# Optimization experiments

Hardware: AMD Instinct MI355X
Metric: run time of the kernel (lower is better)

## Reference

```python
import jax, jax.numpy as jnp
import numpy as np

B, L, D, H, K = 4, 2048, 1024, 16, 256
DH = D // H
SCALE = DH ** -0.5


def setup_inputs() -> dict:
    key = jax.random.key(0)
    ks = jax.random.split(key, 8)
    std = 1.0 / np.sqrt(D)
    pstd = 1.0 / np.sqrt(K)  # init_ uses last dim of (seq_len, k) tensor
    return {
        "x": jax.random.normal(ks[0], (B, L, D), dtype=jnp.float32),
        "Wq": jax.random.uniform(ks[1], (D, D), jnp.float32, -std, std),
        "Wk": jax.random.uniform(ks[2], (D, D), jnp.float32, -std, std),
        "Wv": jax.random.uniform(ks[3], (D, D), jnp.float32, -std, std),
        "proj_k": jax.random.uniform(ks[4], (L, K), jnp.float32, -pstd, pstd),
        "proj_v": jax.random.uniform(ks[5], (L, K), jnp.float32, -pstd, pstd),
        "Wo": jax.random.uniform(ks[6], (D, D), jnp.float32, -std, std),
        "bo": jax.random.uniform(ks[7], (D,), jnp.float32, -std, std),
    }


def reference(x, Wq, Wk, Wv, proj_k, proj_v, Wo, bo):
    b, l, d = x.shape
    q = x @ Wq.T                                   # [B,L,D]
    keys = jnp.einsum("bnd,nk->bkd", x @ Wk.T, proj_k)   # [B,K,D]
    vals = jnp.einsum("bnd,nk->bkd", x @ Wv.T, proj_v)   # [B,K,D]
    # faithful to original: plain reshape (B,h,L,d_h), NOT transpose-split
    q = q.reshape(b, H, l, DH)
    k = keys.reshape(b, K, H, DH).transpose(0, 2, 1, 3)  # [B,H,K,DH]
    v = vals.reshape(b, K, H, DH).transpose(0, 2, 1, 3)  # [B,H,K,DH]
    attn = jax.nn.softmax(jnp.einsum("bhld,bhkd->bhlk", q, k) * SCALE, axis=-1)
    out = jnp.einsum("bhlk,bhkd->bhld", attn, v)
    out = out.transpose(0, 2, 1, 3).reshape(b, l, d)
    return out @ Wo.T + bo
```

## Files before the change

### kernel.cpp

```cpp
#include <hip/hip_runtime.h>


typedef __attribute__((ext_vector_type(8))) short short8;
typedef __attribute__((ext_vector_type(4))) short short4_t;
typedef __attribute__((ext_vector_type(4))) float facc;

#define B_    4
#define L_    2048
#define D_    1024
#define H_    16
#define KP    256
#define DH_   64
#define SCALE_ 0.125f
#define PTS   76

__device__ __forceinline__ short f2b(float f) {
  unsigned u = __float_as_uint(f);
  unsigned r = (u + 0x7fffu + ((u >> 16) & 1u)) >> 16;
  return (short)r;
}

__device__ __forceinline__ void load16_to_lds(const short* gp, short* lp) {
  __builtin_amdgcn_global_load_lds(
      (const __attribute__((address_space(1))) void*)gp,
      (__attribute__((address_space(3))) void*)lp, 16, 0, 0);
}

__global__ __launch_bounds__(256) void prepX(
    const float* __restrict__ x,  const float* __restrict__ pk,
    const float* __restrict__ pv, const float* __restrict__ w0,
    const float* __restrict__ w1, const float* __restrict__ w2,
    const float* __restrict__ w3, short* __restrict__ xb,
    short* __restrict__ xTb, short* __restrict__ projT,
    short* __restrict__ Wb)
{
  const int z = blockIdx.z, tid = threadIdx.x;
  if (z >= 6) {
    const int bid  = blockIdx.y * 32 + blockIdx.x;
    const int widx = (z - 6) * 2 + (bid >> 10);
    const float* s = (widx == 0) ? w0 : (widx == 1) ? w1 : (widx == 2) ? w2 : w3;
    const int i = ((bid & 1023) * 256 + tid) * 4;
    float4 f = *(const float4*)(s + i);
    short4_t v; v[0] = f2b(f.x); v[1] = f2b(f.y); v[2] = f2b(f.z); v[3] = f2b(f.w);
    *(short4_t*)(Wb + (size_t)widx * 1048576 + i) = v;
    return;
  }

  __shared__ float tl[32][37];
  const int row = tid >> 3, c4 = tid & 7;

  if (z < 4) {
    const int b = z, l0 = blockIdx.y * 32, d0 = blockIdx.x * 32;
    const float* s = x + (size_t)b * L_ * D_;
    float4 f = *(const float4*)(s + (size_t)(l0 + row) * D_ + d0 + c4 * 4);
    short4_t v; v[0] = f2b(f.x); v[1] = f2b(f.y); v[2] = f2b(f.z); v[3] = f2b(f.w);
    *(short4_t*)(xb + (size_t)b * L_ * D_ + (size_t)(l0 + row) * D_ + d0 + c4 * 4) = v;
    tl[row][c4 * 4 + 0] = f.x; tl[row][c4 * 4 + 1] = f.y;
    tl[row][c4 * 4 + 2] = f.z; tl[row][c4 * 4 + 3] = f.w;
    __syncthreads();
    short4_t t;
#pragma unroll
    for (int j = 0; j < 4; j++) t[j] = f2b(tl[c4 * 4 + j][row]);
    *(short4_t*)(xTb + (size_t)b * D_ * L_ + (size_t)(d0 + row) * L_ + l0 + c4 * 4) = t;
  } else {
    if (blockIdx.x >= 8) return;
    const int sel = z - 4, l0 = blockIdx.y * 32, k0 = blockIdx.x * 32;
    const float* s = sel ? pv : pk;
    float4 f = *(const float4*)(s + (size_t)(l0 + row) * KP + k0 + c4 * 4);
    tl[row][c4 * 4 + 0] = f.x; tl[row][c4 * 4 + 1] = f.y;
    tl[row][c4 * 4 + 2] = f.z; tl[row][c4 * 4 + 3] = f.w;
    __syncthreads();
    short4_t t;
#pragma unroll
    for (int j = 0; j < 4; j++) t[j] = f2b(tl[c4 * 4 + j][row]);
    *(short4_t*)(projT + (size_t)sel * (KP * L_) + (size_t)(k0 + row) * L_ + l0 + c4 * 4) = t;
  }
}

__global__ __launch_bounds__(512, 2) void gemm8p(
    const short* __restrict__ Am, const short* __restrict__ Bm,
    const float* __restrict__ bias, float* __restrict__ C32,
    short* __restrict__ Cb, int M, int N, int K)
{
  extern __shared__ __attribute__((aligned(16))) short smem[];
  constexpr int BUF  = 24576;
  constexpr int BOFF = 16384;

  const int t = threadIdx.x, lane = t & 63, w = t >> 6;
  const int lm = lane & 15, g = lane >> 4;
  const int bm = blockIdx.x * 4 + (blockIdx.y >> 3);
  const int bn = blockIdx.y & 7;
  const int m0 = bm * 256, n0 = bn * 128;
  const int wm = (w & 3) * 64, wn = (w >> 2) * 64;

  const int srow = lane >> 2;
  const int sslot = lane & 3;

  facc acc[4][4];
  const facc fz = {0.f, 0.f, 0.f, 0.f};
#pragma unroll
  for (int i = 0; i < 4; i++)
#pragma unroll
    for (int j = 0; j < 4; j++) acc[i][j] = fz;

  auto stageA = [&](int kt, int buf, int rnd) {
    const int task = rnd * 8 + w;
    const int c = task >> 4, grp = task & 15;
    const int row = grp * 16 + srow;
    const int slot = sslot ^ ((row >> 1) & 3);
    load16_to_lds(Am + (size_t)(m0 + row) * K + kt * 64 + c * 32 + slot * 8,
                  smem + buf * BUF + c * 8192 + grp * 512);
  };
  auto stageB = [&](int kt, int buf, int rnd) {
    const int task = rnd * 8 + w;
    const int c = task >> 3, grp = task & 7;
    const int row = grp * 16 + srow;
    const int slot = sslot ^ ((row >> 1) & 3);
    load16_to_lds(Bm + (size_t)(n0 + row) * K + kt * 64 + c * 32 + slot * 8,
                  smem + buf * BUF + BOFF + c * 4096 + grp * 512);
  };

#pragma unroll
  for (int r = 0; r < 4; r++) stageA(0, 0, r);
#pragma unroll
  for (int r = 0; r < 2; r++) stageB(0, 0, r);
#pragma unroll
  for (int r = 0; r < 4; r++) stageA(1, 1, r);
#pragma unroll
  for (int r = 0; r < 2; r++) stageB(1, 1, r);
  asm volatile("s_waitcnt vmcnt(6)" ::: "memory");
  __builtin_amdgcn_sched_barrier(0);
  __builtin_amdgcn_s_barrier();

  const int T = K >> 6;
  int p = 0;
  for (int kt = 0; kt < T; kt++) {
    const int q = (p == 0) ? 2 : p - 1;
    const bool pf = (kt + 2 < T);

#pragma unroll
    for (int c = 0; c < 2; c++) {
      short8 af[4], bf[4];
      const int abase = p * BUF + c * 8192;
      const int bbase = p * BUF + BOFF + c * 4096;
#pragma unroll
      for (int mt = 0; mt < 4; mt++) {
        const int row = wm + 16 * mt + lm;
        af[mt] = *(const short8*)(smem + abase + row * 32 + ((g ^ ((row >> 1) & 3)) * 8));
      }
#pragma unroll
      for (int nt = 0; nt < 4; nt++) {
        const int row = wn + 16 * nt + lm;
        bf[nt] = *(const short8*)(smem + bbase + row * 32 + ((g ^ ((row >> 1) & 3)) * 8));
      }
      if (pf) {
        if (c == 0) { stageA(kt + 2, q, 0); stageA(kt + 2, q, 1); stageB(kt + 2, q, 0); }
        else        { stageA(kt + 2, q, 2); stageA(kt + 2, q, 3); stageB(kt + 2, q, 1); }
      }
      __builtin_amdgcn_s_barrier();
      __builtin_amdgcn_s_setprio(1);
#pragma unroll
      for (int mt = 0; mt < 4; mt++)
#pragma unroll
        for (int nt = 0; nt < 4; nt++)
          acc[mt][nt] = __builtin_amdgcn_mfma_f32_16x16x32_bf16(af[mt], bf[nt], acc[mt][nt], 0, 0, 0);
      __builtin_amdgcn_s_setprio(0);
      if (c == 0) __builtin_amdgcn_s_barrier();
    }

    if (pf) {
      asm volatile("s_waitcnt vmcnt(6)" ::: "memory");
      __builtin_amdgcn_sched_barrier(0);
    } else if (kt + 1 < T) {
      asm volatile("s_waitcnt vmcnt(0)" ::: "memory");
      __builtin_amdgcn_sched_barrier(0);
    }
    __builtin_amdgcn_s_barrier();
    p = (p == 2) ? 0 : p + 1;
  }

#pragma unroll
  for (int mt = 0; mt < 4; mt++)
#pragma unroll
    for (int r = 0; r < 4; r++) {
      const int row = m0 + wm + 16 * mt + 4 * g + r;
#pragma unroll
      for (int nt = 0; nt < 4; nt++) {
        const int col = n0 + wn + 16 * nt + lm;
        float v = acc[mt][nt][r];
        if (bias) v += bias[col];
        if (C32) C32[(size_t)row * N + col] = v;
        if (Cb)  Cb[(size_t)row * N + col] = f2b(v);
      }
    }
}

template<int TM, int TN, int NC, bool SWZ>
__global__ __launch_bounds__(256) void gemm_lds(
    const short* __restrict__ Am, const short* __restrict__ Bm,
    const float* __restrict__ bias, float* __restrict__ C32,
    short* __restrict__ Cb, short* __restrict__ CbT, int M, int N, int K,
    long aHi, long aLo, long bHi, long bLo, long cHi, long cLo, int zDiv)
{
  constexpr int MT = TM / 32, NT = TN / 32;
  __shared__ __attribute__((aligned(16))) short As[NC][TM * 32];
  __shared__ __attribute__((aligned(16))) short Bs[NC][TN * 32];
  const int t = threadIdx.x, lane = t & 63, w = t >> 6;
  const int lm = lane & 15, g = lane >> 4;
  const int z = blockIdx.z, zhi = z / zDiv, zlo = z % zDiv;
  int bm, bn;
  if (SWZ) {
    const int p = blockIdx.y * 8 + blockIdx.x;
    bn = (p >> 3) & 7;
    bm = ((p >> 6) << 3) | (p & 7);
  } else {
    bm = blockIdx.y; bn = blockIdx.x;
  }
  const int m0 = bm * TM, n0 = bn * TN;
  const int wm = (w & 1) * (TM / 2), wn = (w >> 1) * (TN / 2);

  const short* Ab = Am + zhi * aHi + zlo * aLo;
  const short* Bp = Bm + zhi * bHi + zlo * bLo;

  facc acc[MT][NT];
  const facc fz = {0.f, 0.f, 0.f, 0.f};
#pragma unroll
  for (int i = 0; i < MT; i++)
#pragma unroll
    for (int j = 0; j < NT; j++) acc[i][j] = fz;

  const int lrow = lane >> 2;
  const int lch  = (lane & 3) * 8;

  for (int k0 = 0; k0 < K; k0 += 32 * NC) {
    __syncthreads();
#pragma unroll
    for (int c = 0; c < NC; c++) {
#pragma unroll
      for (int rnd = 0; rnd < TM / 64; rnd++) {
        const int row = rnd * 64 + w * 16;
        load16_to_lds(Ab + (size_t)(m0 + row + lrow) * K + k0 + c * 32 + lch,
                      &As[c][row * 32]);
      }
#pragma unroll
      for (int rnd = 0; rnd < TN / 64; rnd++) {
        const int row = rnd * 64 + w * 16;
        load16_to_lds(Bp + (size_t)(n0 + row + lrow) * K + k0 + c * 32 + lch,
                      &Bs[c][row * 32]);
      }
    }
    __syncthreads();

#pragma unroll
    for (int c = 0; c < NC; c++) {
      short8 af[MT], bf[NT];
#pragma unroll
      for (int mt = 0; mt < MT; mt++)
        af[mt] = *(const short8*)(&As[c][(wm + 16 * mt + lm) * 32 + g * 8]);
#pragma unroll
      for (int nt = 0; nt < NT; nt++)
        bf[nt] = *(const short8*)(&Bs[c][(wn + 16 * nt + lm) * 32 + g * 8]);
#pragma unroll
      for (int mt = 0; mt < MT; mt++)
#pragma unroll
        for (int nt = 0; nt < NT; nt++)
          acc[mt][nt] = __builtin_amdgcn_mfma_f32_16x16x32_bf16(af[mt], bf[nt], acc[mt][nt], 0, 0, 0);
    }
  }

  if (CbT && zhi == 1) {
#pragma unroll
    for (int mt = 0; mt < MT; mt++) {
      const int rb = m0 + wm + 16 * mt + 4 * g;
      const size_t bb = (size_t)(rb >> 8) * (16 * 64 * 256);
      const int kp = rb & 255;
#pragma unroll
      for (int nt = 0; nt < NT; nt++) {
        const int col = n0 + wn + 16 * nt + lm;
        short4_t o4;
#pragma unroll
        for (int r = 0; r < 4; r++) o4[r] = f2b(acc[mt][nt][r]);
        *(short4_t*)(CbT + bb + (size_t)col * KP + kp) = o4;
      }
    }
    return;
  }

  const long cz = zhi * cHi + zlo * cLo;
#pragma unroll
  for (int mt = 0; mt < MT; mt++)
#pragma unroll
    for (int r = 0; r < 4; r++) {
      const int row = m0 + wm + 16 * mt + 4 * g + r;
#pragma unroll
      for (int nt = 0; nt < NT; nt++) {
        const int col = n0 + wn + 16 * nt + lm;
        float v = acc[mt][nt][r];
        if (bias) v += bias[col];
        if (C32) C32[cz + (size_t)row * N + col] = v;
        if (Cb)  Cb[cz + (size_t)row * N + col] = f2b(v);
      }
    }
}

__global__ __launch_bounds__(256) void attn_mfma(
    const short* __restrict__ xqb, const short* __restrict__ keysb,
    const short* __restrict__ vTb, short* __restrict__ out2b)
{
  __shared__ __attribute__((aligned(16))) short Kt[2][64 * 72];
  __shared__ __attribute__((aligned(16))) short Vt[2][64 * 72];
  __shared__ __attribute__((aligned(16))) short Pt[4][32 * PTS];

  const int t = threadIdx.x, lane = t & 63, w = t >> 6;
  const int lm = lane & 15, g = lane >> 4;
  const int b = blockIdx.z, h = blockIdx.y;
  const int l0w = blockIdx.x * 128 + w * 32;

  short8 aq[2][2];
#pragma unroll
  for (int mt = 0; mt < 2; mt++) {
    const int l = l0w + 16 * mt + lm;
    const short* qrow = xqb + ((size_t)b * L_ + h * 128 + (l >> 4)) * D_ + (l & 15) * DH_;
#pragma unroll
    for (int ks = 0; ks < 2; ks++)
      aq[mt][ks] = *(const short8*)(qrow + ks * 32 + g * 8);
  }

  facc accO[2][4];
  const facc fz = {0.f, 0.f, 0.f, 0.f};
#pragma unroll
  for (int mt = 0; mt < 2; mt++)
#pragma unroll
    for (int dt = 0; dt < 4; dt++) accO[mt][dt] = fz;
  float lrow[2][4];
#pragma unroll
  for (int mt = 0; mt < 2; mt++)
#pragma unroll
    for (int r = 0; r < 4; r++) lrow[mt][r] = 0.f;

  const short* Kb = keysb + (size_t)b * KP * D_ + h * DH_;
  const short* Vb = vTb + ((size_t)b * H_ + h) * DH_ * KP;

  const int srow = t >> 3, sch = (t & 7) * 8;

#pragma unroll
  for (int i = 0; i < 2; i++) {
    const int row = srow + 32 * i;
    *(short8*)(&Kt[0][row * 72 + sch]) = *(const short8*)(Kb + (size_t)row * D_ + sch);
    *(short8*)(&Vt[0][row * 72 + sch]) = *(const short8*)(Vb + (size_t)row * KP + sch);
  }
  __syncthreads();

  for (int c = 0; c < 4; c++) {
    const int bi = c & 1;

    short8 kr[2], vr[2];
    if (c < 3) {
#pragma unroll
      for (int i = 0; i < 2; i++) {
        const int row = srow + 32 * i;
        kr[i] = *(const short8*)(Kb + (size_t)((c + 1) * 64 + row) * D_ + sch);
        vr[i] = *(const short8*)(Vb + (size_t)row * KP + (c + 1) * 64 + sch);
      }
    }

    facc S[2][4];
#pragma unroll
    for (int mt = 0; mt < 2; mt++)
#pragma unroll
      for (int nt = 0; nt < 4; nt++) S[mt][nt] = fz;
#pragma unroll
    for (int ks = 0; ks < 2; ks++) {
      short8 bk[4];
#pragma unroll
      for (int nt = 0; nt < 4; nt++)
        bk[nt] = *(const short8*)(&Kt[bi][(16 * nt + lm) * 72 + ks * 32 + g * 8]);
#pragma unroll
      for (int mt = 0; mt < 2; mt++)
#pragma unroll
        for (int nt = 0; nt < 4; nt++)
          S[mt][nt] = __builtin_amdgcn_mfma_f32_16x16x32_bf16(aq[mt][ks], bk[nt], S[mt][nt], 0, 0, 0);
    }

    if (c < 3) {
#pragma unroll
      for (int i = 0; i < 2; i++) {
        const int row = srow + 32 * i;
        *(short8*)(&Kt[bi ^ 1][row * 72 + sch]) = kr[i];
        *(short8*)(&Vt[bi ^ 1][row * 72 + sch]) = vr[i];
      }
    }

#pragma unroll
    for (int mt = 0; mt < 2; mt++)
#pragma unroll
      for (int r = 0; r < 4; r++) {
        float ps = 0.f;
        const int prow = (16 * mt + 4 * g + r) * PTS;
#pragma unroll
        for (int nt = 0; nt < 4; nt++) {
          const float p = __expf(S[mt][nt][r] * SCALE_);
          ps += p;
          Pt[w][prow + 16 * nt + lm] = f2b(p);
        }
        lrow[mt][r] += ps;
      }

#pragma unroll
    for (int ks = 0; ks < 2; ks++) {
      short8 ap[2], bv[4];
#pragma unroll
      for (int mt = 0; mt < 2; mt++)
        ap[mt] = *(const short8*)(&Pt[w][(16 * mt + lm) * PTS + ks * 32 + g * 8]);
#pragma unroll
      for (int dt = 0; dt < 4; dt++)
        bv[dt] = *(const short8*)(&Vt[bi][(16 * dt + lm) * 72 + ks * 32 + g * 8]);
#pragma unroll
      for (int mt = 0; mt < 2; mt++)
#pragma unroll
        for (int dt = 0; dt < 4; dt++)
          accO[mt][dt] = __builtin_amdgcn_mfma_f32_16x16x32_bf16(ap[mt], bv[dt], accO[mt][dt], 0, 0, 0);
    }
    __syncthreads();
  }

#pragma unroll
  for (int mt = 0; mt < 2; mt++)
#pragma unroll
    for (int r = 0; r < 4; r++) {
      float ls = lrow[mt][r];
      ls += __shfl_xor(ls, 1);
      ls += __shfl_xor(ls, 2);
      ls += __shfl_xor(ls, 4);
      ls += __shfl_xor(ls, 8);
      const float inv = 1.0f / ls;
      const int l = l0w + 16 * mt + 4 * g + r;
#pragma unroll
      for (int dt = 0; dt < 4; dt++)
        out2b[((size_t)b * L_ + l) * D_ + h * DH_ + 16 * dt + lm] = f2b(accO[mt][dt][r] * inv);
    }
}

extern "C" void kernel_launch(void* const* d_in, const int* in_sizes, int n_in,
                              void* d_out, int out_size, void* d_ws, size_t ws_size,
                              hipStream_t stream)
{
  const float* x      = (const float*)d_in[0];
  const float* Wq     = (const float*)d_in[1];
  const float* Wk     = (const float*)d_in[2];
  const float* Wv     = (const float*)d_in[3];
  const float* proj_k = (const float*)d_in[4];
  const float* proj_v = (const float*)d_in[5];
  const float* Wo     = (const float*)d_in[6];
  const float* bo     = (const float*)d_in[7];
  float* out = (float*)d_out;

  short* ws     = (short*)d_ws;
  short* xqb    = ws;
  short* xTb    = xqb    + 8388608;
  short* xb     = xTb    + 8388608;
  short* out2b  = xb;
  short* Wqb    = xb     + 8388608;
  short* Wkb    = Wqb    + 1048576;
  short* Wvb    = Wkb    + 1048576;
  short* Wob    = Wvb    + 1048576;
  short* projTk = Wob    + 1048576;
  short* projTv = projTk + 524288;
  short* xk2b   = projTv + 524288;
  short* xv2b   = xk2b   + 1048576;
  short* keysb  = xv2b   + 1048576;
  short* valsb  = keysb  + 1048576;
  short* vT     = valsb  + 1048576;
  (void)Wkb; (void)Wvb; (void)projTv; (void)xv2b; (void)valsb;

  static bool attr_set = false;
  if (!attr_set) {
    (void)hipFuncSetAttribute(reinterpret_cast<const void*>(gemm8p),
                              hipFuncAttributeMaxDynamicSharedMemorySize, 147456);
    attr_set = true;
  }

  prepX<<<dim3(32, 64, 8), 256, 0, stream>>>(
      x, proj_k, proj_v, Wq, Wk, Wv, Wo, xb, xTb, projTk, Wqb);

  gemm8p<<<dim3(8, 32, 1), 512, 147456, stream>>>(
      xb, Wqb, nullptr, nullptr, xqb, 8192, 1024, 1024);

  gemm_lds<64, 64, 4, false><<<dim3(16, 4, 8), 256, 0, stream>>>(
      projTk, xTb, nullptr, nullptr, xk2b, nullptr, 256, 1024, 2048,
      524288, 0, 0, (long)D_ * L_, 1048576, 262144, 4);

  gemm_lds<64, 64, 4, false><<<dim3(16, 16, 2), 256, 0, stream>>>(
      xk2b, Wkb, nullptr, nullptr, keysb, vT, 1024, 1024, 1024,
      1048576, 0, 1048576, 0, 0, 0, 1);

  attn_mfma<<<dim3(16, 16, 4), 256, 0, stream>>>(xqb, keysb, vT, out2b);

  gemm8p<<<dim3(8, 32, 1), 512, 147456, stream>>>(
      out2b, Wob, bo, out, nullptr, 8192, 1024, 1024);
}
```

Baseline: 216.4 us.

## Replace sync-per-tile GEMM with triple-buffered prefetch pipeline and swizzled LDS

The templated LDS GEMM used for the Linformer projection and K/V GEMMs is replaced by a 64x64-tile kernel with a three-stage LDS ring buffer. Loads for tile kt+2 are issued while tile kt is computed, using explicit vmcnt waits and a single barrier per iteration. The LDS chunk slot is XOR-swizzled by row to cut bank conflicts, and s_setprio raises wave priority around the MFMA block. The hand-placed waitcnt counts and barriers add some risk of ordering mistakes.

After: 216.0 us, median of 2. No clear change (-0.2%).

```diff
diff --git a/kernel.cpp b/kernel.cpp
--- a/kernel.cpp
+++ b/kernel.cpp
@@ -195,87 +195,96 @@
     }
 }
 
-template<int TM, int TN, int NC, bool SWZ>
-__global__ __launch_bounds__(256) void gemm_lds(
+__global__ __launch_bounds__(256) void gemm_p64(
     const short* __restrict__ Am, const short* __restrict__ Bm,
     const float* __restrict__ bias, float* __restrict__ C32,
     short* __restrict__ Cb, short* __restrict__ CbT, int M, int N, int K,
     long aHi, long aLo, long bHi, long bLo, long cHi, long cLo, int zDiv)
 {
-  constexpr int MT = TM / 32, NT = TN / 32;
-  __shared__ __attribute__((aligned(16))) short As[NC][TM * 32];
-  __shared__ __attribute__((aligned(16))) short Bs[NC][TN * 32];
+  __shared__ __attribute__((aligned(16))) short smem[3 * 8192];
   const int t = threadIdx.x, lane = t & 63, w = t >> 6;
   const int lm = lane & 15, g = lane >> 4;
   const int z = blockIdx.z, zhi = z / zDiv, zlo = z % zDiv;
-  int bm, bn;
-  if (SWZ) {
-    const int p = blockIdx.y * 8 + blockIdx.x;
-    bn = (p >> 3) & 7;
-    bm = ((p >> 6) << 3) | (p & 7);
-  } else {
-    bm = blockIdx.y; bn = blockIdx.x;
-  }
-  const int m0 = bm * TM, n0 = bn * TN;
-  const int wm = (w & 1) * (TM / 2), wn = (w >> 1) * (TN / 2);
+  const int bm = blockIdx.y, bn = blockIdx.x;
+  const int m0 = bm * 64, n0 = bn * 64;
+  const int wm = (w & 1) * 32, wn = (w >> 1) * 32;
 
   const short* Ab = Am + zhi * aHi + zlo * aLo;
   const short* Bp = Bm + zhi * bHi + zlo * bLo;
 
-  facc acc[MT][NT];
+  const int srow = w * 16 + (lane >> 2);
+  const int pslot = (lane & 3) ^ ((srow >> 1) & 3);
+
+  facc acc[2][2];
   const facc fz = {0.f, 0.f, 0.f, 0.f};
 #pragma unroll
-  for (int i = 0; i < MT; i++)
-#pragma unroll
-    for (int j = 0; j < NT; j++) acc[i][j] = fz;
-
-  const int lrow = lane >> 2;
-  const int lch  = (lane & 3) * 8;
-
-  for (int k0 = 0; k0 < K; k0 += 32 * NC) {
-    __syncthreads();
-#pragma unroll
-    for (int c = 0; c < NC; c++) {
-#pragma unroll
-      for (int rnd = 0; rnd < TM / 64; rnd++) {
-        const int row = rnd * 64 + w * 16;
-        load16_to_lds(Ab + (size_t)(m0 + row + lrow) * K + k0 + c * 32 + lch,
-                      &As[c][row * 32]);
-      }
-#pragma unroll
-      for (int rnd = 0; rnd < TN / 64; rnd++) {
-        const int row = rnd * 64 + w * 16;
-        load16_to_lds(Bp + (size_t)(n0 + row + lrow) * K + k0 + c * 32 + lch,
-                      &Bs[c][row * 32]);
-      }
-    }
-    __syncthreads();
-
-#pragma unroll
-    for (int c = 0; c < NC; c++) {
-      short8 af[MT], bf[NT];
-#pragma unroll
-      for (int mt = 0; mt < MT; mt++)
-        af[mt] = *(const short8*)(&As[c][(wm + 16 * mt + lm) * 32 + g * 8]);
-#pragma unroll
-      for (int nt = 0; nt < NT; nt++)
-        bf[nt] = *(const short8*)(&Bs[c][(wn + 16 * nt + lm) * 32 + g * 8]);
-#pragma unroll
-      for (int mt = 0; mt < MT; mt++)
-#pragma unroll
-        for (int nt = 0; nt < NT; nt++)
+  for (int i = 0; i < 2; i++)
+#pragma unroll
+    for (int j = 0; j < 2; j++) acc[i][j] = fz;
+
+  auto stage_h = [&](int kt, int buf, int c) {
+    load16_to_lds(Ab + (size_t)(m0 + srow) * K + kt * 64 + c * 32 + pslot * 8,
+                  smem + buf * 8192 + c * 2048 + w * 512);
+    load16_to_lds(Bp + (size_t)(n0 + srow) * K + kt * 64 + c * 32 + pslot * 8,
+                  smem + buf * 8192 + 4096 + c * 2048 + w * 512);
+  };
+
+  stage_h(0, 0, 0); stage_h(0, 0, 1);
+  stage_h(1, 1, 0); stage_h(1, 1, 1);
+  asm volatile("s_waitcnt vmcnt(4)" ::: "memory");
+  __builtin_amdgcn_sched_barrier(0);
+  __builtin_amdgcn_s_barrier();
+
+  const int T = K >> 6;
+  int p = 0;
+  for (int kt = 0; kt < T; kt++) {
+    const int q = (p == 0) ? 2 : p - 1;
+    const bool pf = (kt + 2 < T);
+
+#pragma unroll
+    for (int c = 0; c < 2; c++) {
+      short8 af[2], bf[2];
+      const int abase = p * 8192 + c * 2048;
+      const int bbase = p * 8192 + 4096 + c * 2048;
+#pragma unroll
+      for (int mt = 0; mt < 2; mt++) {
+        const int row = wm + 16 * mt + lm;
+        af[mt] = *(const short8*)(smem + abase + row * 32 + ((g ^ ((row >> 1) & 3)) * 8));
+      }
+#pragma unroll
+      for (int nt = 0; nt < 2; nt++) {
+        const int row = wn + 16 * nt + lm;
+        bf[nt] = *(const short8*)(smem + bbase + row * 32 + ((g ^ ((row >> 1) & 3)) * 8));
+      }
+      if (pf) stage_h(kt + 2, q, c);
+      __builtin_amdgcn_s_setprio(1);
+#pragma unroll
+      for (int mt = 0; mt < 2; mt++)
+#pragma unroll
+        for (int nt = 0; nt < 2; nt++)
           acc[mt][nt] = __builtin_amdgcn_mfma_f32_16x16x32_bf16(af[mt], bf[nt], acc[mt][nt], 0, 0, 0);
-    }
+      __builtin_amdgcn_s_setprio(0);
+    }
+
+    if (pf) {
+      asm volatile("s_waitcnt vmcnt(4)" ::: "memory");
+      __builtin_amdgcn_sched_barrier(0);
+    } else if (kt + 1 < T) {
+      asm volatile("s_waitcnt vmcnt(0)" ::: "memory");
+      __builtin_amdgcn_sched_barrier(0);
+    }
+    __builtin_amdgcn_s_barrier();
+    p = (p == 2) ? 0 : p + 1;
   }
 
   if (CbT && zhi == 1) {
 #pragma unroll
-    for (int mt = 0; mt < MT; mt++) {
+    for (int mt = 0; mt < 2; mt++) {
       const int rb = m0 + wm + 16 * mt + 4 * g;
       const size_t bb = (size_t)(rb >> 8) * (16 * 64 * 256);
       const int kp = rb & 255;
 #pragma unroll
-      for (int nt = 0; nt < NT; nt++) {
+      for (int nt = 0; nt < 2; nt++) {
         const int col = n0 + wn + 16 * nt + lm;
         short4_t o4;
 #pragma unroll
@@ -288,12 +297,12 @@
 
   const long cz = zhi * cHi + zlo * cLo;
 #pragma unroll
-  for (int mt = 0; mt < MT; mt++)
+  for (int mt = 0; mt < 2; mt++)
 #pragma unroll
     for (int r = 0; r < 4; r++) {
       const int row = m0 + wm + 16 * mt + 4 * g + r;
 #pragma unroll
-      for (int nt = 0; nt < NT; nt++) {
+      for (int nt = 0; nt < 2; nt++) {
         const int col = n0 + wn + 16 * nt + lm;
         float v = acc[mt][nt][r];
         if (bias) v += bias[col];
@@ -486,11 +495,11 @@
   gemm8p<<<dim3(8, 32, 1), 512, 147456, stream>>>(
       xb, Wqb, nullptr, nullptr, xqb, 8192, 1024, 1024);
 
-  gemm_lds<64, 64, 4, false><<<dim3(16, 4, 8), 256, 0, stream>>>(
+  gemm_p64<<<dim3(16, 4, 8), 256, 0, stream>>>(
       projTk, xTb, nullptr, nullptr, xk2b, nullptr, 256, 1024, 2048,
       524288, 0, 0, (long)D_ * L_, 1048576, 262144, 4);
 
-  gemm_lds<64, 64, 4, false><<<dim3(16, 16, 2), 256, 0, stream>>>(
+  gemm_p64<<<dim3(16, 16, 2), 256, 0, stream>>>(
       xk2b, Wkb, nullptr, nullptr, keysb, vT, 1024, 1024, 1024,
       1048576, 0, 1048576, 0, 0, 0, 1);
 
```
